# Kernel tuning notes

Hardware: AMD Instinct MI355X
Metric: run time of the kernel (lower is better)

Reference implementation:

```python
import jax, jax.numpy as jnp
import numpy as np

B, IN, OUT = 2048, 64, 2048


def setup_inputs() -> dict:
    key = jax.random.key(0)
    k1, k2, k3 = jax.random.split(key, 3)
    x = jax.random.normal(k1, (B, IN), dtype=jnp.float32)
    # learned params (shapes per init: means [in, out], inv_std_dev [out, in, in])
    means = jax.random.uniform(k2, (IN, OUT), dtype=jnp.float32)
    # roughly like the inverse of a diagonal step matrix plus small noise
    inv_std_dev = (jax.random.normal(k3, (OUT, IN, IN), dtype=jnp.float32) * 0.05
                   + jnp.eye(IN, dtype=jnp.float32) * 0.5)
    return {"x": x, "means": means, "inv_std_dev": inv_std_dev}


def reference(x, means, inv_std_dev):
    # diff[b, o, i] = x[b, i] - means[i, o]   -> [B, OUT, IN]
    d = x[:, None, :] - means.T[None, :, :]
    # torch uses inv_std_dev.pow(2) (elementwise square), not a matrix square
    A = inv_std_dev * inv_std_dev  # [OUT, IN, IN]
    # per-neuron quadratic form: q[b, o] = d[b,o,:] @ A[o] @ d[b,o,:]
    q = jnp.einsum('boi,oij,boj->bo', d, A, d)
    return jnp.exp(-0.5 * q)  # [B, OUT]
```

## Files before the change

kernel.cpp:

```cpp
#include <hip/hip_runtime.h>
#include <hip/hip_bf16.h>

typedef __bf16 bf16x8 __attribute__((ext_vector_type(8)));
typedef float f32x4 __attribute__((ext_vector_type(4)));
typedef float f32x16 __attribute__((ext_vector_type(16)));
typedef int i32x4 __attribute__((ext_vector_type(4)));

#define B_N 2048
#define O_N 2048
#define K_N 64

__global__ __launch_bounds__(256) void rbf_prep(
    const float* __restrict__ inv, const float* __restrict__ means,
    __bf16* __restrict__ Atp, unsigned int* __restrict__ cPack,
    float* __restrict__ kArr)
{
    __shared__ float s[64 * 65];
    __shared__ float mld[64];
    __shared__ float uw[128];
    const int o = blockIdx.x;
    const int t = threadIdx.x;
    const float4* src = (const float4*)(inv + (size_t)o * 4096);
#pragma unroll
    for (int k = 0; k < 4; ++k) {
        const int idx = k * 256 + t;
        const float4 v = src[idx];
        const int i = idx >> 4;
        const int j0 = (idx & 15) * 4;
        s[i * 65 + j0 + 0] = v.x * v.x;
        s[i * 65 + j0 + 1] = v.y * v.y;
        s[i * 65 + j0 + 2] = v.z * v.z;
        s[i * 65 + j0 + 3] = v.w * v.w;
    }
    if (t < 64) mld[t] = means[(size_t)t * O_N + o];
    __syncthreads();
    if (t < 64) {
        float u = 0.f;
#pragma unroll
        for (int i = 0; i < 64; ++i) u = fmaf(s[i * 65 + t], mld[i], u);
        uw[t] = u;
    } else if (t < 128) {
        const int j = t - 64;
        float w = 0.f;
#pragma unroll
        for (int i = 0; i < 64; ++i) w = fmaf(s[j * 65 + i], mld[i], w);
        uw[64 + j] = w;
    }
    __syncthreads();
    if (t < 64) {
        const float c = -(uw[t] + uw[64 + t]);
        const __bf16 hi = (__bf16)c;
        const __bf16 lo = (__bf16)(c - (float)hi);
        const unsigned int hb = __builtin_bit_cast(unsigned short, hi);
        const unsigned int lb = __builtin_bit_cast(unsigned short, lo);
        cPack[(size_t)o * 64 + t] = hb | (lb << 16);
    }
    if (t == 0) {
        float kk = 0.f;
#pragma unroll
        for (int j = 0; j < 64; ++j) kk = fmaf(uw[j], mld[j], kk);
        kArr[o] = kk;
    }
#pragma unroll
    for (int r = 0; r < 2; ++r) {
        const int ch = r * 256 + t;
        const int ss = ch >> 7;
        const int j = (ch >> 1) & 63;
        const int h = ch & 1;
        bf16x8 v;
#pragma unroll
        for (int e = 0; e < 8; ++e)
            v[e] = (__bf16)s[(16 * ss + 8 * h + e) * 65 + j];
        *(bf16x8*)(Atp + (size_t)o * 4096 + (size_t)ch * 8) = v;
    }
}

__global__ __launch_bounds__(256, 3) void rbf_main(
    const float* __restrict__ x, const __bf16* __restrict__ Atp,
    const unsigned int* __restrict__ cPack, const float* __restrict__ kArr,
    float* __restrict__ out)
{
    __shared__ __align__(16) __bf16 sA[2][4096];

    const int tid = threadIdx.x;
    const int wave = tid >> 6;
    const int lane = tid & 63;
    const int b = lane & 31;
    const int h = lane >> 5;

    const int wg = (int)blockIdx.x;
    const int xcd = wg & 7;
    const int loc = wg >> 3;
    const int og = xcd * 8 + (loc >> 4);
    const int bg = loc & 15;
    const int oBase = og * 32;
    const int rowW = bg * 128 + wave * 32;
    const int row = rowW + b;
    const float* xr = x + (size_t)row * K_N;

    bf16x8 xb[4];
#pragma unroll
    for (int ss = 0; ss < 4; ++ss) {
        const float4 a = *(const float4*)(xr + ss * 16 + h * 8);
        const float4 bb = *(const float4*)(xr + ss * 16 + h * 8 + 4);
        bf16x8 v;
        v[0] = (__bf16)a.x;  v[1] = (__bf16)a.y;
        v[2] = (__bf16)a.z;  v[3] = (__bf16)a.w;
        v[4] = (__bf16)bb.x; v[5] = (__bf16)bb.y;
        v[6] = (__bf16)bb.z; v[7] = (__bf16)bb.w;
        xb[ss] = v;
    }
    f32x4 xd[2][4];
#pragma unroll
    for (int mt = 0; mt < 2; ++mt)
#pragma unroll
        for (int rq = 0; rq < 4; ++rq)
            xd[mt][rq] = *(const f32x4*)(xr + mt * 32 + rq * 8 + h * 4);

    const i32x4 onesI = { h ? 0 : 0x3F803F80, 0, 0, 0 };
    const bf16x8 onesF = __builtin_bit_cast(bf16x8, onesI);
    const f32x16 zz = {0.f,0.f,0.f,0.f,0.f,0.f,0.f,0.f,
                       0.f,0.f,0.f,0.f,0.f,0.f,0.f,0.f};

    const bf16x8* gA = (const bf16x8*)Atp;
    bf16x8 st0, st1;
    st0 = gA[(size_t)oBase * 512 + tid];
    st1 = gA[(size_t)oBase * 512 + 256 + tid];
    ((bf16x8*)sA[0])[tid] = st0;
    ((bf16x8*)sA[0])[256 + tid] = st1;

    float q4[4];

#pragma unroll 4
    for (int i = 0; i < 32; ++i) {
        __syncthreads();
        if (i < 31) {
            const size_t gbase = (size_t)(oBase + i + 1) * 512;
            st0 = gA[gbase + tid];
            st1 = gA[gbase + 256 + tid];
        }
        const __bf16* bufp = sA[i & 1];

        const unsigned int cw0 = cPack[(size_t)(oBase + i) * 64 + b];
        const unsigned int cw1 = cPack[(size_t)(oBase + i) * 64 + 32 + b];
        const float kk = kArr[oBase + i];
        const i32x4 c0i = { h ? 0 : (int)cw0, 0, 0, 0 };
        const i32x4 c1i = { h ? 0 : (int)cw1, 0, 0, 0 };
        const bf16x8 cf0 = __builtin_bit_cast(bf16x8, c0i);
        const bf16x8 cf1 = __builtin_bit_cast(bf16x8, c1i);

        f32x16 acc0 = zz, acc1 = zz;
#pragma unroll
        for (int ss = 0; ss < 4; ++ss) {
            const bf16x8 af0 = *(const bf16x8*)(bufp + ss * 1024 + b * 16 + h * 8);
            acc0 = __builtin_amdgcn_mfma_f32_32x32x16_bf16(af0, xb[ss], acc0, 0, 0, 0);
        }
#pragma unroll
        for (int ss = 0; ss < 4; ++ss) {
            const bf16x8 af1 = *(const bf16x8*)(bufp + ss * 1024 + (32 + b) * 16 + h * 8);
            acc1 = __builtin_amdgcn_mfma_f32_32x32x16_bf16(af1, xb[ss], acc1, 0, 0, 0);
        }
        acc0 = __builtin_amdgcn_mfma_f32_32x32x16_bf16(cf0, onesF, acc0, 0, 0, 0);
        acc1 = __builtin_amdgcn_mfma_f32_32x32x16_bf16(cf1, onesF, acc1, 0, 0, 0);

        float q = 0.f;
#pragma unroll
        for (int rg = 0; rg < 4; ++rg)
#pragma unroll
            for (int e = 0; e < 4; ++e)
                q = fmaf(acc0[rg * 4 + e], xd[0][rg][e], q);
#pragma unroll
        for (int rg = 0; rg < 4; ++rg)
#pragma unroll
            for (int e = 0; e < 4; ++e)
                q = fmaf(acc1[rg * 4 + e], xd[1][rg][e], q);
        q += __shfl_xor(q, 32, 64);
        const float ev = exp2f((q + kk) * -0.72134752044448170368f);
        q4[i & 3] = ev;

        if ((i & 3) == 3 && h == 0) {
            const f32x4 v = {q4[0], q4[1], q4[2], q4[3]};
            *(f32x4*)(out + (size_t)row * O_N + oBase + (i - 3)) = v;
        }
        if (i < 31) {
            ((bf16x8*)sA[(i + 1) & 1])[tid] = st0;
            ((bf16x8*)sA[(i + 1) & 1])[256 + tid] = st1;
        }
    }
}

extern "C" void kernel_launch(void* const* d_in, const int* in_sizes, int n_in,
                              void* d_out, int out_size, void* d_ws, size_t ws_size,
                              hipStream_t stream)
{
    const float* x = (const float*)d_in[0];
    const float* means = (const float*)d_in[1];
    const float* inv = (const float*)d_in[2];
    float* out = (float*)d_out;

    __bf16* Atp = (__bf16*)d_ws;
    unsigned int* cPack = (unsigned int*)((char*)d_ws + (size_t)O_N * 4096 * sizeof(__bf16));
    float* kArr = (float*)((char*)cPack + (size_t)O_N * 64 * sizeof(unsigned int));

    rbf_prep<<<dim3(O_N), dim3(256), 0, stream>>>(inv, means, Atp, cPack, kArr);
    rbf_main<<<dim3(1024), dim3(256), 0, stream>>>(x, Atp, cPack, kArr, out);

    (void)in_sizes; (void)n_in; (void)out_size; (void)ws_size;
}
```

Baseline: 70.07 us.

## Precompute linear term via split-bf16 MFMA and stream A tiles with global_load_lds

```diff
diff --git a/kernel.cpp b/kernel.cpp
--- a/kernel.cpp
+++ b/kernel.cpp
@@ -4,16 +4,22 @@
 typedef __bf16 bf16x8 __attribute__((ext_vector_type(8)));
 typedef float f32x4 __attribute__((ext_vector_type(4)));
 typedef float f32x16 __attribute__((ext_vector_type(16)));
-typedef int i32x4 __attribute__((ext_vector_type(4)));
 
 #define B_N 2048
 #define O_N 2048
 #define K_N 64
 
+__device__ __forceinline__ void gld16(const void* g, void* l) {
+    __builtin_amdgcn_global_load_lds(
+        (const __attribute__((address_space(1))) void*)g,
+        (__attribute__((address_space(3))) void*)l,
+        16, 0, 0);
+}
+
 __global__ __launch_bounds__(256) void rbf_prep(
     const float* __restrict__ inv, const float* __restrict__ means,
-    __bf16* __restrict__ Atp, unsigned int* __restrict__ cPack,
-    float* __restrict__ kArr)
+    __bf16* __restrict__ Atp, __bf16* __restrict__ cPhi,
+    __bf16* __restrict__ cPlo, float* __restrict__ kArr)
 {
     __shared__ float s[64 * 65];
     __shared__ float mld[64];
@@ -51,9 +57,10 @@
         const float c = -(uw[t] + uw[64 + t]);
         const __bf16 hi = (__bf16)c;
         const __bf16 lo = (__bf16)(c - (float)hi);
-        const unsigned int hb = __builtin_bit_cast(unsigned short, hi);
-        const unsigned int lb = __builtin_bit_cast(unsigned short, lo);
-        cPack[(size_t)o * 64 + t] = hb | (lb << 16);
+        const size_t eidx = (size_t)(o >> 5) * 2048 + (size_t)(t >> 4) * 512
+                          + (size_t)(o & 31) * 16 + (t & 15);
+        cPhi[eidx] = hi;
+        cPlo[eidx] = lo;
     }
     if (t == 0) {
         float kk = 0.f;
@@ -75,12 +82,14 @@
     }
 }
 
-__global__ __launch_bounds__(256, 3) void rbf_main(
+__global__ __launch_bounds__(256, 4) void rbf_main(
     const float* __restrict__ x, const __bf16* __restrict__ Atp,
-    const unsigned int* __restrict__ cPack, const float* __restrict__ kArr,
-    float* __restrict__ out)
+    const __bf16* __restrict__ cPhi, const __bf16* __restrict__ cPlo,
+    const float* __restrict__ kArr, float* __restrict__ out)
 {
     __shared__ __align__(16) __bf16 sA[2][4096];
+    __shared__ __align__(16) float sLin[4][32][32];
+    __shared__ float sK[32];
 
     const int tid = threadIdx.x;
     const int wave = tid >> 6;
@@ -98,17 +107,22 @@
     const int row = rowW + b;
     const float* xr = x + (size_t)row * K_N;
 
-    bf16x8 xb[4];
+    const f32x16 zz = {0.f,0.f,0.f,0.f,0.f,0.f,0.f,0.f,
+                       0.f,0.f,0.f,0.f,0.f,0.f,0.f,0.f};
+
+    bf16x8 xh[4], xl[4];
 #pragma unroll
     for (int ss = 0; ss < 4; ++ss) {
-        const float4 a = *(const float4*)(xr + ss * 16 + h * 8);
-        const float4 bb = *(const float4*)(xr + ss * 16 + h * 8 + 4);
-        bf16x8 v;
-        v[0] = (__bf16)a.x;  v[1] = (__bf16)a.y;
-        v[2] = (__bf16)a.z;  v[3] = (__bf16)a.w;
-        v[4] = (__bf16)bb.x; v[5] = (__bf16)bb.y;
-        v[6] = (__bf16)bb.z; v[7] = (__bf16)bb.w;
-        xb[ss] = v;
+        const float* p = xr + ss * 16 + h * 8;
+        bf16x8 vh, vl;
+#pragma unroll
+        for (int e = 0; e < 8; ++e) {
+            const float v = p[e];
+            const __bf16 hi = (__bf16)v;
+            vh[e] = hi;
+            vl[e] = (__bf16)(v - (float)hi);
+        }
+        xh[ss] = vh; xl[ss] = vl;
     }
     f32x4 xd[2][4];
 #pragma unroll
@@ -117,74 +131,78 @@
         for (int rq = 0; rq < 4; ++rq)
             xd[mt][rq] = *(const f32x4*)(xr + mt * 32 + rq * 8 + h * 4);
 
-    const i32x4 onesI = { h ? 0 : 0x3F803F80, 0, 0, 0 };
-    const bf16x8 onesF = __builtin_bit_cast(bf16x8, onesI);
-    const f32x16 zz = {0.f,0.f,0.f,0.f,0.f,0.f,0.f,0.f,
-                       0.f,0.f,0.f,0.f,0.f,0.f,0.f,0.f};
-
-    const bf16x8* gA = (const bf16x8*)Atp;
-    bf16x8 st0, st1;
-    st0 = gA[(size_t)oBase * 512 + tid];
-    st1 = gA[(size_t)oBase * 512 + 256 + tid];
-    ((bf16x8*)sA[0])[tid] = st0;
-    ((bf16x8*)sA[0])[256 + tid] = st1;
+    {
+        const __bf16* ch = cPhi + (size_t)og * 2048;
+        const __bf16* cl = cPlo + (size_t)og * 2048;
+        f32x16 lin = zz;
+#pragma unroll
+        for (int ss = 0; ss < 4; ++ss) {
+            const bf16x8 fh = *(const bf16x8*)(ch + ss * 512 + b * 16 + h * 8);
+            const bf16x8 fl = *(const bf16x8*)(cl + ss * 512 + b * 16 + h * 8);
+            lin = __builtin_amdgcn_mfma_f32_32x32x16_bf16(fh, xh[ss], lin, 0, 0, 0);
+            lin = __builtin_amdgcn_mfma_f32_32x32x16_bf16(fh, xl[ss], lin, 0, 0, 0);
+            lin = __builtin_amdgcn_mfma_f32_32x32x16_bf16(fl, xh[ss], lin, 0, 0, 0);
+        }
+#pragma unroll
+        for (int r = 0; r < 16; ++r)
+            sLin[wave][(r & 3) + 8 * (r >> 2) + 4 * h][b] = lin[r];
+    }
+    if (tid < 32) sK[tid] = kArr[oBase + tid];
+
+    const int L0 = tid * 16;
+    const int L1 = 4096 + tid * 16;
+    const int S0 = L0 ^ (((L0 >> 7) & 7) << 4);
+    const int S1 = L1 ^ (((L1 >> 7) & 7) << 4);
+    const char* gp = (const char*)(Atp + (size_t)oBase * 4096);
+    gld16(gp + S0, (char*)&sA[0][0] + L0);
+    gld16(gp + S1, (char*)&sA[0][0] + L1);
+
+    const int off0 = (b * 32 + h * 16) ^ (((b >> 2) & 7) << 4);
 
     float q4[4];
-
 #pragma unroll 4
     for (int i = 0; i < 32; ++i) {
         __syncthreads();
         if (i < 31) {
-            const size_t gbase = (size_t)(oBase + i + 1) * 512;
-            st0 = gA[gbase + tid];
-            st1 = gA[gbase + 256 + tid];
-        }
-        const __bf16* bufp = sA[i & 1];
-
-        const unsigned int cw0 = cPack[(size_t)(oBase + i) * 64 + b];
-        const unsigned int cw1 = cPack[(size_t)(oBase + i) * 64 + 32 + b];
-        const float kk = kArr[oBase + i];
-        const i32x4 c0i = { h ? 0 : (int)cw0, 0, 0, 0 };
-        const i32x4 c1i = { h ? 0 : (int)cw1, 0, 0, 0 };
-        const bf16x8 cf0 = __builtin_bit_cast(bf16x8, c0i);
-        const bf16x8 cf1 = __builtin_bit_cast(bf16x8, c1i);
+            const char* gn = gp + (size_t)(i + 1) * 8192;
+            char* ld = (char*)&sA[(i + 1) & 1][0];
+            gld16(gn + S0, ld + L0);
+            gld16(gn + S1, ld + L1);
+        }
+        const char* bufp = (const char*)&sA[i & 1][0];
 
         f32x16 acc0 = zz, acc1 = zz;
 #pragma unroll
         for (int ss = 0; ss < 4; ++ss) {
-            const bf16x8 af0 = *(const bf16x8*)(bufp + ss * 1024 + b * 16 + h * 8);
-            acc0 = __builtin_amdgcn_mfma_f32_32x32x16_bf16(af0, xb[ss], acc0, 0, 0, 0);
+            const bf16x8 a0 = *(const bf16x8*)(bufp + ss * 2048 + off0);
+            acc0 = __builtin_amdgcn_mfma_f32_32x32x16_bf16(a0, xh[ss], acc0, 0, 0, 0);
         }
 #pragma unroll
         for (int ss = 0; ss < 4; ++ss) {
-            const bf16x8 af1 = *(const bf16x8*)(bufp + ss * 1024 + (32 + b) * 16 + h * 8);
-            acc1 = __builtin_amdgcn_mfma_f32_32x32x16_bf16(af1, xb[ss], acc1, 0, 0, 0);
-        }
-        acc0 = __builtin_amdgcn_mfma_f32_32x32x16_bf16(cf0, onesF, acc0, 0, 0, 0);
-        acc1 = __builtin_amdgcn_mfma_f32_32x32x16_bf16(cf1, onesF, acc1, 0, 0, 0);
-
-        float q = 0.f;
+            const bf16x8 a1 = *(const bf16x8*)(bufp + ss * 2048 + 1024 + off0);
+            acc1 = __builtin_amdgcn_mfma_f32_32x32x16_bf16(a1, xh[ss], acc1, 0, 0, 0);
+        }
+
+        float p[4] = {0.f, 0.f, 0.f, 0.f};
 #pragma unroll
         for (int rg = 0; rg < 4; ++rg)
 #pragma unroll
             for (int e = 0; e < 4; ++e)
-                q = fmaf(acc0[rg * 4 + e], xd[0][rg][e], q);
+                p[rg] = fmaf(acc0[rg * 4 + e], xd[0][rg][e], p[rg]);
 #pragma unroll
         for (int rg = 0; rg < 4; ++rg)
 #pragma unroll
             for (int e = 0; e < 4; ++e)
-                q = fmaf(acc1[rg * 4 + e], xd[1][rg][e], q);
+                p[rg] = fmaf(acc1[rg * 4 + e], xd[1][rg][e], p[rg]);
+        float q = (p[0] + p[1]) + (p[2] + p[3]);
         q += __shfl_xor(q, 32, 64);
-        const float ev = exp2f((q + kk) * -0.72134752044448170368f);
+        q += sLin[wave][i][b];
+        const float ev = exp2f((q + sK[i]) * -0.72134752044448170368f);
         q4[i & 3] = ev;
 
         if ((i & 3) == 3 && h == 0) {
             const f32x4 v = {q4[0], q4[1], q4[2], q4[3]};
             *(f32x4*)(out + (size_t)row * O_N + oBase + (i - 3)) = v;
-        }
-        if (i < 31) {
-            ((bf16x8*)sA[(i + 1) & 1])[tid] = st0;
-            ((bf16x8*)sA[(i + 1) & 1])[256 + tid] = st1;
         }
     }
 }
@@ -198,12 +216,14 @@
     const float* inv = (const float*)d_in[2];
     float* out = (float*)d_out;
 
-    __bf16* Atp = (__bf16*)d_ws;
-    unsigned int* cPack = (unsigned int*)((char*)d_ws + (size_t)O_N * 4096 * sizeof(__bf16));
-    float* kArr = (float*)((char*)cPack + (size_t)O_N * 64 * sizeof(unsigned int));
-
-    rbf_prep<<<dim3(O_N), dim3(256), 0, stream>>>(inv, means, Atp, cPack, kArr);
-    rbf_main<<<dim3(1024), dim3(256), 0, stream>>>(x, Atp, cPack, kArr, out);
+    char* w = (char*)d_ws;
+    __bf16* Atp  = (__bf16*)w;
+    __bf16* cPhi = (__bf16*)(w + (size_t)O_N * 4096 * 2);
+    __bf16* cPlo = (__bf16*)(w + (size_t)O_N * 4096 * 2 + 262144);
+    float*  kArr = (float*)(w + (size_t)O_N * 4096 * 2 + 524288);
+
+    rbf_prep<<<dim3(O_N), dim3(256), 0, stream>>>(inv, means, Atp, cPhi, cPlo, kArr);
+    rbf_main<<<dim3(1024), dim3(256), 0, stream>>>(x, Atp, cPhi, cPlo, kArr, out);
 
     (void)in_sizes; (void)n_in; (void)out_size; (void)ws_size;
 }
```

Result: faster. 64.54 us (-7.9%).
